# Kernel optimization log

Hardware: AMD Instinct MI355X
Metric: run time of the kernel (lower is better)

The kernel has to match this reference:

```python
import jax, jax.numpy as jnp
import numpy as np


def setup_inputs() -> dict:
    key = jax.random.key(0)
    ks = jax.random.split(key, 8)
    N, C, T, V = 32, 64, 256, 25
    OUT, INTER, S = 64, 16, 3
    W_SCALE = 0.05  # keep complex softmax exp() well-conditioned
    return {
        "x_real": jax.random.normal(ks[0], (N, C, T, V), jnp.float32),
        "x_imag": jax.random.normal(ks[1], (N, C, T, V), jnp.float32),
        "A": jax.random.uniform(ks[2], (S, V, V), jnp.float32),
        "PA": jax.random.normal(ks[3], (S, V, V), jnp.float32) * 1e-3,
        "Wa": jax.random.normal(ks[4], (S, 2 * INTER, 2 * C), jnp.float32) * W_SCALE,
        "ba": jnp.zeros((S, 2 * INTER), jnp.float32),
        "Wb": jax.random.normal(ks[5], (S, 2 * INTER, 2 * C), jnp.float32) * W_SCALE,
        "bb": jnp.zeros((S, 2 * INTER), jnp.float32),
        "Wd": jax.random.normal(ks[6], (S, 2 * OUT, 2 * C), jnp.float32) * W_SCALE,
        "bd": jnp.zeros((S, 2 * OUT), jnp.float32),
        "bn_weight": jnp.ones((OUT,), jnp.float32),
        "bn_bias": jnp.zeros((OUT,), jnp.float32),
    }


def _cconv1x1(z, W, b):
    # C_Conv2d with k=1: 1x1 conv over concat(real, imag) channels.
    zc = jnp.concatenate([z.real, z.imag], axis=1)          # [N, 2*Cin, T, V]
    o = jnp.einsum("oc,nctv->notv", W, zc) + b[None, :, None, None]
    h = W.shape[0] // 2
    return jax.lax.complex(o[:, :h], o[:, h:])              # [N, Cout, T, V] complex


def _forward(x_real, x_imag, A, PA, Wa, ba, Wb, bb, Wd, bd, bn_weight, bn_bias):
    x = jax.lax.complex(x_real, x_imag)                     # [N, C, T, V]
    N, C, T, V = x.shape
    inter = Wa.shape[1] // 2
    Afull = A + PA                                          # [3, V, V] real
    X2 = x.reshape(N, C * T, V)
    y = None
    for i in range(A.shape[0]):
        A1 = _cconv1x1(x, Wa[i], ba[i])                     # [N, inter, T, V]
        A1 = A1.transpose(0, 3, 1, 2).reshape(N, V, inter * T)
        A2 = _cconv1x1(x, Wb[i], bb[i]).reshape(N, inter * T, V)
        S = jnp.matmul(A1, A2) / (inter * T)                # [N, V, V] complex
        # complex softmax over dim=1 (no max-subtraction, faithful to C_softmax)
        ez = jnp.exp(S)
        S = ez / jnp.sum(ez, axis=1, keepdims=True)
        S = S + Afull[i]
        z = jnp.matmul(X2, S).reshape(N, C, T, V)
        z = _cconv1x1(z, Wd[i], bd[i])                      # [N, OUT, T, V]
        y = z if y is None else y + z
    # C_BatchNorm2d on complex input: complex mean, real variance = E|y-mu|^2
    mu = jnp.mean(y, axis=(0, 2, 3))                        # [OUT] complex
    var = jnp.mean(jnp.abs(y - mu[None, :, None, None]) ** 2, axis=(0, 2, 3))
    yn = (y - mu[None, :, None, None]) / jnp.sqrt(var + 1e-5)[None, :, None, None]
    yn = yn * bn_weight[None, :, None, None] + bn_bias[None, :, None, None]
    yn = yn + x  # down = identity (in_channels == out_channels)
    return jnp.stack([yn.real, yn.imag])                    # [2, N, OUT, T, V] real


def reference(x_real, x_imag, A, PA, Wa, ba, Wb, bb, Wd, bd, bn_weight, bn_bias):
    return _forward(x_real, x_imag, A, PA, Wa, ba, Wb, bb, Wd, bd, bn_weight, bn_bias)
```

## Files before the change

### kernel.cpp

```cpp
#include <hip/hip_runtime.h>
#include <hip/hip_bf16.h>
#include <stdint.h>

#define NN 32
#define CC 64
#define TTOT 256
#define VV 25
#define NS 3
constexpr int TV  = TTOT * VV;
constexpr int CTV = CC * TV;
constexpr size_t PLANE = (size_t)NN * CTV;

typedef unsigned short ushort_t;
using short8 = __attribute__((ext_vector_type(8))) short;
using f32x4  = __attribute__((ext_vector_type(4))) float;

static __device__ __forceinline__ ushort_t f2bf(float f) {
  __hip_bfloat16 h = __float2bfloat16(f);
  return reinterpret_cast<ushort_t&>(h);
}
static __device__ __forceinline__ float bf2f(ushort_t h) {
  union { uint32_t u; float f; } v; v.u = ((uint32_t)h) << 16;
  return v.f;
}
static __device__ __forceinline__ int SWZ(int row, int k) {
  return ((row << 7) + k) ^ ((row & 7) << 3);
}
static __device__ __forceinline__ f32x4 mfma16(short8 a, short8 b, f32x4 c) {
  return __builtin_amdgcn_mfma_f32_16x16x32_bf16(a, b, c, 0, 0, 0);
}
static __device__ __forceinline__ short8 negbf8(short8 x) {
  short8 r;
#pragma unroll
  for (int j = 0; j < 8; ++j) r[j] = x[j] ^ (short)0x8000;
  return r;
}

__global__ __launch_bounds__(256) void k0_wfrag(
    const float* __restrict__ Wd, const float* __restrict__ Wa,
    const float* __restrict__ Wb, ushort_t* __restrict__ wfrag,
    ushort_t* __restrict__ wab)
{
  const int i = blockIdx.x;
  for (int e = threadIdx.x; e < 16384; e += 256) {
    int ot = e >> 11, m = (e >> 9) & 3, l = (e >> 3) & 63, j = e & 7;
    int r  = ot * 16 + (l & 15);
    int c = m * 16 + ((l >> 4) << 2) + (j >> 1), comp = j & 1;
    wfrag[(size_t)i * 16384 + e] = f2bf(Wd[(size_t)i * 16384 + r * 128 + comp * 64 + c]);
  }
  for (int e = threadIdx.x; e < 8192; e += 256) {
    int mt = e >> 11, ks = (e >> 9) & 3, l = (e >> 3) & 63, j = e & 7;
    int r  = mt * 16 + (l & 15);
    int kp = ks * 32 + ((l >> 4) << 3) + j;
    float v = (r < 32) ? Wa[((size_t)i * 32 + r) * 128 + kp]
                       : Wb[((size_t)i * 32 + (r - 32)) * 128 + kp];
    wab[(size_t)i * 8192 + e] = f2bf(v);
  }
}

__global__ __launch_bounds__(256) void k1_spart(
    const float* __restrict__ xr, const float* __restrict__ xi,
    const ushort_t* __restrict__ wab, const float* __restrict__ ba,
    const float* __restrict__ bb, float* __restrict__ Spart)
{
  const int tc = blockIdx.x, n = blockIdx.y;
  const int tid = threadIdx.x, lane = tid & 63, wv = tid >> 6;
  const int r16 = lane & 15, gw = lane >> 4;
  __shared__ alignas(16) ushort_t zc[128 * 128];
  __shared__ alignas(16) ushort_t Ga[NS][32 * 128];
  __shared__ alignas(16) ushort_t Gb[NS][32 * 128];

  for (int e4 = tid; e4 < 128 * 25; e4 += 256) {
    int c = e4 / 25, q = e4 % 25;
    const float* src = (c < 64) ? xr : xi;
    float4 w = *(const float4*)&src[(size_t)n * CTV + (c & 63) * TV + tc * 100 + q * 4];
#pragma unroll
    for (int jj = 0; jj < 4; ++jj) {
      int g = q * 4 + jj, t = g / 25, v = g - t * 25;
      zc[SWZ(t * 32 + v, c)] = f2bf(((const float*)&w)[jj]);
    }
  }
  for (int e = tid; e < 28 * 128; e += 256) {
    int r7 = e >> 7, c = e & 127;
    int t = r7 / 7, vv = 25 + r7 % 7;
    zc[SWZ(t * 32 + vv, c)] = 0;
  }
  __syncthreads();

#pragma unroll 1
  for (int i = 0; i < NS; ++i) {
    short8 afr[4];
#pragma unroll
    for (int ks = 0; ks < 4; ++ks)
      afr[ks] = *(const short8*)&wab[((((size_t)i * 4 + wv) * 4 + ks) * 64 + lane) * 8];
    float bias[4];
#pragma unroll
    for (int j = 0; j < 4; ++j) {
      int row = wv * 16 + gw * 4 + j;
      bias[j] = (row < 32) ? ba[i * 32 + row] : bb[i * 32 + (row - 32)];
    }
    ushort_t* gbuf = (wv < 2) ? Ga[i] : Gb[i];
    const int half = (wv & 1) * 64;
    for (int nt = 0; nt < 8; ++nt) {
      f32x4 acc = {0.f, 0.f, 0.f, 0.f};
      const int brow = nt * 16 + r16;
#pragma unroll
      for (int ks = 0; ks < 4; ++ks) {
        short8 bfr = *(const short8*)&zc[SWZ(brow, ks * 32 + gw * 8)];
        acc = mfma16(afr[ks], bfr, acc);
      }
      int pos2 = nt * 16 + r16;
      int t = pos2 >> 5, v = pos2 & 31;
      int k0w = half + t * 16 + gw * 4;
      uint32_t w0 = (uint32_t)f2bf(acc[0] + bias[0]) | ((uint32_t)f2bf(acc[1] + bias[1]) << 16);
      uint32_t w1 = (uint32_t)f2bf(acc[2] + bias[2]) | ((uint32_t)f2bf(acc[3] + bias[3]) << 16);
      uint2 pk; pk.x = w0; pk.y = w1;
      *(uint2*)&gbuf[SWZ(v, k0w)] = pk;
    }
  }
  __syncthreads();

  const int mu = wv >> 1, nv = wv & 1;
  const int urow = mu * 16 + r16;
  const int vrow = nv * 16 + r16;
#pragma unroll 1
  for (int i = 0; i < NS; ++i) {
    f32x4 Prr = {0.f,0.f,0.f,0.f}, Pii = {0.f,0.f,0.f,0.f};
    f32x4 Pri = {0.f,0.f,0.f,0.f}, Pir = {0.f,0.f,0.f,0.f};
#pragma unroll
    for (int ks = 0; ks < 2; ++ks) {
      int ko = ks * 32 + gw * 8;
      short8 arF = *(const short8*)&Ga[i][SWZ(urow, ko)];
      short8 aiF = *(const short8*)&Ga[i][SWZ(urow, 64 + ko)];
      short8 brF = *(const short8*)&Gb[i][SWZ(vrow, ko)];
      short8 biF = *(const short8*)&Gb[i][SWZ(vrow, 64 + ko)];
      Prr = mfma16(arF, brF, Prr);
      Pii = mfma16(aiF, biF, Pii);
      Pri = mfma16(arF, biF, Pri);
      Pir = mfma16(aiF, brF, Pir);
    }
#pragma unroll
    for (int j = 0; j < 4; ++j) {
      int u = mu * 16 + gw * 4 + j;
      int v = nv * 16 + r16;
      if (u < VV && v < VV) {
        size_t idx = ((((size_t)i * NN + n) * 64 + tc) * 625 + u * 25 + v) * 2;
        Spart[idx]     = Prr[j] - Pii[j];
        Spart[idx + 1] = Pri[j] + Pir[j];
      }
    }
  }
}

__global__ __launch_bounds__(256) void k2_softmax(
    const float* __restrict__ Spart, const float* __restrict__ Aw,
    const float* __restrict__ PA, ushort_t* __restrict__ sfrag)
{
  const int i = blockIdx.x, n = blockIdx.y, tid = threadIdx.x;
  __shared__ float ez[625 * 2];
  __shared__ float den[25 * 2];
  for (int e = tid; e < 625; e += 256) {
    float sr = 0.f, si = 0.f;
    const float* p = Spart + (((size_t)i * NN + n) * 64 * 625 + e) * 2;
    for (int tcb = 0; tcb < 64; ++tcb) { sr += p[0]; si += p[1]; p += 625 * 2; }
    sr *= (1.f / 4096.f); si *= (1.f / 4096.f);
    float m = expf(sr);
    ez[e * 2] = m * cosf(si);
    ez[e * 2 + 1] = m * sinf(si);
  }
  __syncthreads();
  if (tid < 25) {
    float dr = 0.f, di = 0.f;
    for (int u = 0; u < 25; ++u) { dr += ez[(u * 25 + tid) * 2]; di += ez[(u * 25 + tid) * 2 + 1]; }
    float inv = 1.f / (dr * dr + di * di);
    den[tid * 2] = dr * inv; den[tid * 2 + 1] = -di * inv;
  }
  __syncthreads();
  for (int e = tid; e < 625; e += 256) {
    int v = e % 25;
    float er = ez[e * 2], ei = ez[e * 2 + 1];
    float dr = den[v * 2], di = den[v * 2 + 1];
    float outr = er * dr - ei * di + Aw[i * 625 + e] + PA[i * 625 + e];
    float outi = er * di + ei * dr;
    ez[e * 2] = outr; ez[e * 2 + 1] = outi;
  }
  __syncthreads();
  for (int e = tid; e < 256; e += 256) {
    int l = e & 63, nt = (e >> 6) & 1, m = e >> 7;
    int u0 = (l >> 4) << 3, v = nt * 16 + (l & 15);
    short8 pk;
#pragma unroll
    for (int j = 0; j < 8; ++j) {
      int u = u0 + j;
      float val = 0.f;
      if (u < VV && v < VV)
        val = (m == 0) ? ez[(u * 25 + v) * 2] : ez[(u * 25 + v) * 2 + 1];
      pk[j] = (short)f2bf(val);
    }
    *(short8*)&sfrag[((size_t)(i * NN + n) * 256 + e) * 8] = pk;
  }
}

__global__ __launch_bounds__(512) void k3_y(
    const float* __restrict__ xr, const float* __restrict__ xi,
    const ushort_t* __restrict__ sfrag, const ushort_t* __restrict__ wfrag,
    const float* __restrict__ bd, float* __restrict__ out,
    float* __restrict__ bnpart)
{
  const int tq8 = blockIdx.x, n = blockIdx.y;
  const int tid = threadIdx.x, lane = tid & 63, wv = tid >> 6;
  const int r16 = lane & 15, gw = lane >> 4;
  __shared__ alignas(16) ushort_t wlds[49152];
  __shared__ float stats[8][128][2];

  {
    ushort_t* xs = wlds;
    for (int e4 = tid; e4 < 128 * 50; e4 += 512) {
      int c = e4 / 50, q = e4 % 50;
      const float* src = (c < 64) ? xr : xi;
      float4 w = *(const float4*)&src[(size_t)n * CTV + (c & 63) * TV + tq8 * 200 + q * 4];
#pragma unroll
      for (int jj = 0; jj < 4; ++jj) {
        int g = q * 4 + jj, t = g / 25, u = g - t * 25;
        xs[(t >> 2) * 16384 + SWZ(c, (t & 3) * 32 + u)] = f2bf(((const float*)&w)[jj]);
      }
    }
    for (int e = tid; e < 128 * 56; e += 512) {
      int c = e / 56, r = e % 56;
      int t = r / 7, u = 25 + r % 7;
      xs[(t >> 2) * 16384 + SWZ(c, (t & 3) * 32 + u)] = 0;
    }
  }
  __syncthreads();

  const int tl = wv & 3, th = wv >> 2;
  const int kx = tl * 32 + gw * 8;
  short8 axr[4], axi[4];
#pragma unroll
  for (int tile = 0; tile < 4; ++tile) {
    axr[tile] = *(const short8*)&wlds[th * 16384 + SWZ(tile * 16 + r16, kx)];
    axi[tile] = *(const short8*)&wlds[th * 16384 + SWZ(64 + tile * 16 + r16, kx)];
  }
  __syncthreads();

  {
    short8 tmp[12];
#pragma unroll
    for (int q = 0; q < 12; ++q)
      tmp[q] = *(const short8*)&wfrag[(size_t)(q * 512 + tid) * 8];
#pragma unroll
    for (int q = 0; q < 12; ++q)
      *(short8*)&wlds[(size_t)(q * 512 + tid) * 8] = tmp[q];
  }
  __syncthreads();

  f32x4 acc[8][2];
#pragma unroll
  for (int a = 0; a < 8; ++a) { acc[a][0] = {0.f,0.f,0.f,0.f}; acc[a][1] = {0.f,0.f,0.f,0.f}; }

  auto load_sf = [&](int i, short8 sf[2][2]) {
    const ushort_t* sb = sfrag + (size_t)(i * NN + n) * 2048;
#pragma unroll
    for (int m = 0; m < 2; ++m)
#pragma unroll
      for (int nt = 0; nt < 2; ++nt)
        sf[m][nt] = *(const short8*)&sb[((m * 2 + nt) * 64 + lane) * 8];
  };
  auto compute_i = [&](int i, short8 sf[2][2]) {
    short8 snI[2];
#pragma unroll
    for (int nt = 0; nt < 2; ++nt) snI[nt] = negbf8(sf[1][nt]);
    short8 bp[4][2];
#pragma unroll
    for (int tile = 0; tile < 4; ++tile) {
#pragma unroll
      for (int nt = 0; nt < 2; ++nt) {
        f32x4 zr = {0.f,0.f,0.f,0.f}, zi = {0.f,0.f,0.f,0.f};
        zr = mfma16(axr[tile], sf[0][nt], zr);
        zr = mfma16(axi[tile], snI[nt], zr);
        zi = mfma16(axr[tile], sf[1][nt], zi);
        zi = mfma16(axi[tile], sf[0][nt], zi);
        short8 pk;
#pragma unroll
        for (int j = 0; j < 4; ++j) {
          pk[2 * j]     = (short)f2bf(zr[j]);
          pk[2 * j + 1] = (short)f2bf(zi[j]);
        }
        bp[tile][nt] = pk;
      }
    }
#pragma unroll
    for (int ot = 0; ot < 8; ++ot) {
#pragma unroll
      for (int m = 0; m < 4; ++m) {
        short8 a = *(const short8*)&wlds[((size_t)i * 16384) + (size_t)((ot * 4 + m) * 64 + lane) * 8];
        acc[ot][0] = mfma16(a, bp[m][0], acc[ot][0]);
        acc[ot][1] = mfma16(a, bp[m][1], acc[ot][1]);
      }
    }
  };

  short8 sfA[2][2], sfB[2][2];
  load_sf(0, sfA);
  load_sf(1, sfB);
  compute_i(0, sfA);
  load_sf(2, sfA);
  compute_i(1, sfB);
  compute_i(2, sfA);

  const int t = tq8 * 8 + wv;
#pragma unroll
  for (int ot = 0; ot < 8; ++ot) {
#pragma unroll
    for (int j = 0; j < 4; ++j) {
      int row = ot * 16 + gw * 4 + j;
      float bias = bd[row] + bd[128 + row] + bd[256 + row];
      float s = 0.f, q = 0.f;
#pragma unroll
      for (int nt = 0; nt < 2; ++nt) {
        int v = nt * 16 + r16;
        float val = acc[ot][nt][j] + bias;
        if (v < VV) {
          out[(size_t)(row >> 6) * PLANE + (size_t)n * CTV + (row & 63) * TV + t * VV + v] = val;
          s += val; q += val * val;
        }
      }
#pragma unroll
      for (int d = 1; d < 16; d <<= 1) { s += __shfl_xor(s, d); q += __shfl_xor(q, d); }
      if (r16 == 0) { stats[wv][row][0] = s; stats[wv][row][1] = q; }
    }
  }
  __syncthreads();
  if (tid < 128) {
    float s = 0.f, q = 0.f;
#pragma unroll
    for (int w = 0; w < 8; ++w) { s += stats[w][tid][0]; q += stats[w][tid][1]; }
    size_t b = (size_t)n * 32 + tq8;
    bnpart[(b * 128 + tid) * 2]     = s;
    bnpart[(b * 128 + tid) * 2 + 1] = q;
  }
}

__global__ __launch_bounds__(256) void k4_stats(
    const float* __restrict__ bnpart, const float* __restrict__ bnw,
    const float* __restrict__ bnb, float* __restrict__ coeff)
{
  const int o = blockIdx.x, tid = threadIdx.x;
  float sr = 0.f, qr = 0.f, si = 0.f, qi = 0.f;
  for (int b = tid; b < 1024; b += 256) {
    const float* p = bnpart + ((size_t)b * 128 + o) * 2;
    sr += p[0]; qr += p[1];
    const float* p2 = bnpart + ((size_t)b * 128 + 64 + o) * 2;
    si += p2[0]; qi += p2[1];
  }
#pragma unroll
  for (int d = 1; d < 64; d <<= 1) {
    sr += __shfl_xor(sr, d); qr += __shfl_xor(qr, d);
    si += __shfl_xor(si, d); qi += __shfl_xor(qi, d);
  }
  __shared__ float red[4][4];
  int lane = tid & 63, wv = tid >> 6;
  if (lane == 0) { red[wv][0] = sr; red[wv][1] = qr; red[wv][2] = si; red[wv][3] = qi; }
  __syncthreads();
  if (tid == 0) {
    sr = red[0][0] + red[1][0] + red[2][0] + red[3][0];
    qr = red[0][1] + red[1][1] + red[2][1] + red[3][1];
    si = red[0][2] + red[1][2] + red[2][2] + red[3][2];
    qi = red[0][3] + red[1][3] + red[2][3] + red[3][3];
    const float invM = 1.f / (float)((size_t)NN * TTOT * VV);
    float mur = sr * invM, mui = si * invM;
    float var = (qr + qi) * invM - mur * mur - mui * mui;
    float inv = rsqrtf(var + 1e-5f);
    coeff[o * 4 + 0] = mur; coeff[o * 4 + 1] = mui;
    coeff[o * 4 + 2] = inv * bnw[o]; coeff[o * 4 + 3] = bnb[o];
  }
}

__global__ __launch_bounds__(256) void k5_norm(
    const float* __restrict__ xr, const float* __restrict__ xi,
    const float* __restrict__ coeff, float* __restrict__ out)
{
  size_t idx0 = ((size_t)blockIdx.x * 256 + threadIdx.x) * 4;
  size_t stride = (size_t)gridDim.x * 256 * 4;
  for (size_t e = idx0; e < PLANE; e += stride) {
    int o = (int)((e / TV) & 63);
    float4 cf = *(const float4*)&coeff[o * 4];
    float4 yr = *(float4*)&out[e];
    float4 yi = *(float4*)&out[PLANE + e];
    float4 vr = *(const float4*)&xr[e];
    float4 vi = *(const float4*)&xi[e];
    yr.x = (yr.x - cf.x) * cf.z + cf.w + vr.x;
    yr.y = (yr.y - cf.x) * cf.z + cf.w + vr.y;
    yr.z = (yr.z - cf.x) * cf.z + cf.w + vr.z;
    yr.w = (yr.w - cf.x) * cf.z + cf.w + vr.w;
    yi.x = (yi.x - cf.y) * cf.z + vi.x;
    yi.y = (yi.y - cf.y) * cf.z + vi.y;
    yi.z = (yi.z - cf.y) * cf.z + vi.z;
    yi.w = (yi.w - cf.y) * cf.z + vi.w;
    *(float4*)&out[e] = yr;
    *(float4*)&out[PLANE + e] = yi;
  }
}

extern "C" void kernel_launch(void* const* d_in, const int* in_sizes, int n_in,
                              void* d_out, int out_size, void* d_ws, size_t ws_size,
                              hipStream_t stream) {
  const float* xr  = (const float*)d_in[0];
  const float* xi  = (const float*)d_in[1];
  const float* Aw  = (const float*)d_in[2];
  const float* PA  = (const float*)d_in[3];
  const float* Wa  = (const float*)d_in[4];
  const float* ba  = (const float*)d_in[5];
  const float* Wb  = (const float*)d_in[6];
  const float* bb  = (const float*)d_in[7];
  const float* Wd  = (const float*)d_in[8];
  const float* bd  = (const float*)d_in[9];
  const float* bnw = (const float*)d_in[10];
  const float* bnb = (const float*)d_in[11];
  float* out = (float*)d_out;
  float* ws = (float*)d_ws;

  float*    Spart  = ws;
  float*    bnpart = ws;
  ushort_t* sfrag  = (ushort_t*)(ws + 7680000);
  ushort_t* wfrag  = (ushort_t*)(ws + 7778304);
  ushort_t* wab    = (ushort_t*)(ws + 7802880);
  float*    coeff  = ws + 7815168;

  k0_wfrag<<<NS, 256, 0, stream>>>(Wd, Wa, Wb, wfrag, wab);
  k1_spart<<<dim3(64, NN), 256, 0, stream>>>(xr, xi, wab, ba, bb, Spart);
  k2_softmax<<<dim3(NS, NN), 256, 0, stream>>>(Spart, Aw, PA, sfrag);
  k3_y<<<dim3(32, NN), 512, 0, stream>>>(xr, xi, sfrag, wfrag, bd, out, bnpart);
  k4_stats<<<64, 256, 0, stream>>>(bnpart, bnw, bnb, coeff);
  k5_norm<<<6400, 256, 0, stream>>>(xr, xi, coeff, out);
}
```

Before: 247.1 us.

## Split k3 output channels across blocks to shrink LDS and raise occupancy

The y-kernel now uses 256-thread blocks, each handling 4 time steps and one half (real or imaginary) of the 128 output rows, giving four times as many blocks. LDS use drops from about 96KB to about 48KB per block and the accumulator array is halved, so more blocks can be resident per CU. The swizzled x layout is replaced by a padded row stride of 40, and the MFMA loop is wrapped in s_setprio. The cost is that each block reloads x and recomputes the complex S-multiply that the other half-block also computes. The BN partial layout and k4 reduction are adjusted to match.

```diff
diff --git a/kernel.cpp b/kernel.cpp
--- a/kernel.cpp
+++ b/kernel.cpp
@@ -201,62 +201,66 @@
   }
 }
 
-__global__ __launch_bounds__(512) void k3_y(
+__global__ __launch_bounds__(256) void k3_y(
     const float* __restrict__ xr, const float* __restrict__ xi,
     const ushort_t* __restrict__ sfrag, const ushort_t* __restrict__ wfrag,
     const float* __restrict__ bd, float* __restrict__ out,
     float* __restrict__ bnpart)
 {
-  const int tq8 = blockIdx.x, n = blockIdx.y;
+  const int tq4 = blockIdx.x >> 1, h = blockIdx.x & 1, n = blockIdx.y;
   const int tid = threadIdx.x, lane = tid & 63, wv = tid >> 6;
   const int r16 = lane & 15, gw = lane >> 4;
-  __shared__ alignas(16) ushort_t wlds[49152];
-  __shared__ float stats[8][128][2];
+  __shared__ alignas(16) ushort_t smem[24576];
+  __shared__ float stats[4][64][2];
+
+  for (int e4 = tid; e4 < 128 * 25; e4 += 256) {
+    int c = e4 / 25, q = e4 % 25;
+    const float* src = (c < 64) ? xr : xi;
+    float4 w = *(const float4*)&src[(size_t)n * CTV + (size_t)(c & 63) * TV + tq4 * 100 + q * 4];
+#pragma unroll
+    for (int jj = 0; jj < 4; ++jj) {
+      int g = q * 4 + jj, t = g / 25, u = g - t * 25;
+      smem[t * 5120 + c * 40 + u] = f2bf(((const float*)&w)[jj]);
+    }
+  }
+  for (int e = tid; e < 128 * 28; e += 256) {
+    int c = e / 28, r = e % 28;
+    int t = r / 7, u = 25 + r % 7;
+    smem[t * 5120 + c * 40 + u] = 0;
+  }
+  __syncthreads();
+
+  short8 axr[4], axi[4];
+#pragma unroll
+  for (int tile = 0; tile < 4; ++tile) {
+    int cr = tile * 16 + r16;
+    axr[tile] = *(const short8*)&smem[wv * 5120 + cr * 40 + gw * 8];
+    axi[tile] = *(const short8*)&smem[wv * 5120 + (64 + cr) * 40 + gw * 8];
+  }
+  __syncthreads();
 
   {
-    ushort_t* xs = wlds;
-    for (int e4 = tid; e4 < 128 * 50; e4 += 512) {
-      int c = e4 / 50, q = e4 % 50;
-      const float* src = (c < 64) ? xr : xi;
-      float4 w = *(const float4*)&src[(size_t)n * CTV + (c & 63) * TV + tq8 * 200 + q * 4];
-#pragma unroll
-      for (int jj = 0; jj < 4; ++jj) {
-        int g = q * 4 + jj, t = g / 25, u = g - t * 25;
-        xs[(t >> 2) * 16384 + SWZ(c, (t & 3) * 32 + u)] = f2bf(((const float*)&w)[jj]);
-      }
-    }
-    for (int e = tid; e < 128 * 56; e += 512) {
-      int c = e / 56, r = e % 56;
-      int t = r / 7, u = 25 + r % 7;
-      xs[(t >> 2) * 16384 + SWZ(c, (t & 3) * 32 + u)] = 0;
-    }
-  }
-  __syncthreads();
-
-  const int tl = wv & 3, th = wv >> 2;
-  const int kx = tl * 32 + gw * 8;
-  short8 axr[4], axi[4];
-#pragma unroll
-  for (int tile = 0; tile < 4; ++tile) {
-    axr[tile] = *(const short8*)&wlds[th * 16384 + SWZ(tile * 16 + r16, kx)];
-    axi[tile] = *(const short8*)&wlds[th * 16384 + SWZ(64 + tile * 16 + r16, kx)];
-  }
-  __syncthreads();
-
-  {
-    short8 tmp[12];
-#pragma unroll
-    for (int q = 0; q < 12; ++q)
-      tmp[q] = *(const short8*)&wfrag[(size_t)(q * 512 + tid) * 8];
-#pragma unroll
-    for (int q = 0; q < 12; ++q)
-      *(short8*)&wlds[(size_t)(q * 512 + tid) * 8] = tmp[q];
-  }
-  __syncthreads();
-
-  f32x4 acc[8][2];
-#pragma unroll
-  for (int a = 0; a < 8; ++a) { acc[a][0] = {0.f,0.f,0.f,0.f}; acc[a][1] = {0.f,0.f,0.f,0.f}; }
+    short8 tmp[6];
+#pragma unroll
+    for (int b = 0; b < 2; ++b) {
+#pragma unroll
+      for (int q = 0; q < 6; ++q) {
+        int e = (b * 6 + q) * 256 + tid;
+        int i = e >> 10, local = e & 1023;
+        tmp[q] = *(const short8*)&wfrag[(size_t)i * 16384 + h * 8192 + (size_t)local * 8];
+      }
+#pragma unroll
+      for (int q = 0; q < 6; ++q) {
+        int e = (b * 6 + q) * 256 + tid;
+        *(short8*)&smem[(size_t)e * 8] = tmp[q];
+      }
+    }
+  }
+  __syncthreads();
+
+  f32x4 acc[4][2];
+#pragma unroll
+  for (int a = 0; a < 4; ++a) { acc[a][0] = {0.f,0.f,0.f,0.f}; acc[a][1] = {0.f,0.f,0.f,0.f}; }
 
   auto load_sf = [&](int i, short8 sf[2][2]) {
     const ushort_t* sb = sfrag + (size_t)(i * NN + n) * 2048;
@@ -289,15 +293,17 @@
         bp[tile][nt] = pk;
       }
     }
-#pragma unroll
-    for (int ot = 0; ot < 8; ++ot) {
+    __builtin_amdgcn_s_setprio(1);
+#pragma unroll
+    for (int otl = 0; otl < 4; ++otl) {
 #pragma unroll
       for (int m = 0; m < 4; ++m) {
-        short8 a = *(const short8*)&wlds[((size_t)i * 16384) + (size_t)((ot * 4 + m) * 64 + lane) * 8];
-        acc[ot][0] = mfma16(a, bp[m][0], acc[ot][0]);
-        acc[ot][1] = mfma16(a, bp[m][1], acc[ot][1]);
-      }
-    }
+        short8 a = *(const short8*)&smem[(size_t)i * 8192 + (size_t)((otl * 4 + m) * 64 + lane) * 8];
+        acc[otl][0] = mfma16(a, bp[m][0], acc[otl][0]);
+        acc[otl][1] = mfma16(a, bp[m][1], acc[otl][1]);
+      }
+    }
+    __builtin_amdgcn_s_setprio(0);
   };
 
   short8 sfA[2][2], sfB[2][2];
@@ -308,36 +314,36 @@
   compute_i(1, sfB);
   compute_i(2, sfA);
 
-  const int t = tq8 * 8 + wv;
-#pragma unroll
-  for (int ot = 0; ot < 8; ++ot) {
+  const int t = tq4 * 4 + wv;
+#pragma unroll
+  for (int otl = 0; otl < 4; ++otl) {
 #pragma unroll
     for (int j = 0; j < 4; ++j) {
-      int row = ot * 16 + gw * 4 + j;
+      int lrow = otl * 16 + gw * 4 + j;
+      int row = h * 64 + lrow;
       float bias = bd[row] + bd[128 + row] + bd[256 + row];
       float s = 0.f, q = 0.f;
 #pragma unroll
       for (int nt = 0; nt < 2; ++nt) {
         int v = nt * 16 + r16;
-        float val = acc[ot][nt][j] + bias;
+        float val = acc[otl][nt][j] + bias;
         if (v < VV) {
-          out[(size_t)(row >> 6) * PLANE + (size_t)n * CTV + (row & 63) * TV + t * VV + v] = val;
+          out[(size_t)h * PLANE + (size_t)n * CTV + (row & 63) * TV + t * VV + v] = val;
           s += val; q += val * val;
         }
       }
 #pragma unroll
       for (int d = 1; d < 16; d <<= 1) { s += __shfl_xor(s, d); q += __shfl_xor(q, d); }
-      if (r16 == 0) { stats[wv][row][0] = s; stats[wv][row][1] = q; }
-    }
-  }
-  __syncthreads();
-  if (tid < 128) {
-    float s = 0.f, q = 0.f;
-#pragma unroll
-    for (int w = 0; w < 8; ++w) { s += stats[w][tid][0]; q += stats[w][tid][1]; }
-    size_t b = (size_t)n * 32 + tq8;
-    bnpart[(b * 128 + tid) * 2]     = s;
-    bnpart[(b * 128 + tid) * 2 + 1] = q;
+      if (r16 == 0) { stats[wv][lrow][0] = s; stats[wv][lrow][1] = q; }
+    }
+  }
+  __syncthreads();
+  if (tid < 64) {
+    float s = stats[0][tid][0] + stats[1][tid][0] + stats[2][tid][0] + stats[3][tid][0];
+    float q = stats[0][tid][1] + stats[1][tid][1] + stats[2][tid][1] + stats[3][tid][1];
+    size_t b = (size_t)n * 64 + tq4;
+    bnpart[((b * 2 + h) * 64 + tid) * 2]     = s;
+    bnpart[((b * 2 + h) * 64 + tid) * 2 + 1] = q;
   }
 }
 
@@ -347,10 +353,10 @@
 {
   const int o = blockIdx.x, tid = threadIdx.x;
   float sr = 0.f, qr = 0.f, si = 0.f, qi = 0.f;
-  for (int b = tid; b < 1024; b += 256) {
-    const float* p = bnpart + ((size_t)b * 128 + o) * 2;
+  for (int b = tid; b < 2048; b += 256) {
+    const float* p = bnpart + ((size_t)(b * 2 + 0) * 64 + o) * 2;
     sr += p[0]; qr += p[1];
-    const float* p2 = bnpart + ((size_t)b * 128 + 64 + o) * 2;
+    const float* p2 = bnpart + ((size_t)(b * 2 + 1) * 64 + o) * 2;
     si += p2[0]; qi += p2[1];
   }
 #pragma unroll
@@ -430,7 +436,7 @@
   k0_wfrag<<<NS, 256, 0, stream>>>(Wd, Wa, Wb, wfrag, wab);
   k1_spart<<<dim3(64, NN), 256, 0, stream>>>(xr, xi, wab, ba, bb, Spart);
   k2_softmax<<<dim3(NS, NN), 256, 0, stream>>>(Spart, Aw, PA, sfrag);
-  k3_y<<<dim3(32, NN), 512, 0, stream>>>(xr, xi, sfrag, wfrag, bd, out, bnpart);
+  k3_y<<<dim3(128, NN), 256, 0, stream>>>(xr, xi, sfrag, wfrag, bd, out, bnpart);
   k4_stats<<<64, 256, 0, stream>>>(bnpart, bnw, bnb, coeff);
   k5_norm<<<6400, 256, 0, stream>>>(xr, xi, coeff, out);
 }
```

Result: slower. 254.6 us (+3.0%).

## Split softmax partial-sum reduction into a wide pre-reduce kernel; raise MFMA wave priority

Applied to the files above, without the earlier changes.

The 64-way reduction of S partials, previously done serially per element by only 96 blocks, is split into a new k2a_reduce kernel that runs 768 blocks, each summing 8 partials. The softmax kernel then only sums 8. This spreads a latency-bound serial reduction over many more CUs, at the cost of an extra launch and an intermediate buffer. Separately, k3_y raises wave priority around its MFMA accumulation loop with s_setprio.

```diff
diff --git a/kernel.cpp b/kernel.cpp
--- a/kernel.cpp
+++ b/kernel.cpp
@@ -152,17 +152,35 @@
   }
 }
 
-__global__ __launch_bounds__(256) void k2_softmax(
-    const float* __restrict__ Spart, const float* __restrict__ Aw,
+__global__ __launch_bounds__(256) void k2a_reduce(
+    const float* __restrict__ Spart, float* __restrict__ Spart2)
+{
+  const int chunk = blockIdx.x, in = blockIdx.y, tid = threadIdx.x;
+  const float* base = Spart + ((size_t)in * 64 + chunk * 8) * 1250;
+  float* outp = Spart2 + ((size_t)in * 8 + chunk) * 1250;
+  for (int e = tid; e < 1250; e += 256) {
+    float s = 0.f;
+#pragma unroll
+    for (int k = 0; k < 8; ++k) s += base[(size_t)k * 1250 + e];
+    outp[e] = s;
+  }
+}
+
+__global__ __launch_bounds__(256) void k2b_softmax(
+    const float* __restrict__ Spart2, const float* __restrict__ Aw,
     const float* __restrict__ PA, ushort_t* __restrict__ sfrag)
 {
   const int i = blockIdx.x, n = blockIdx.y, tid = threadIdx.x;
   __shared__ float ez[625 * 2];
   __shared__ float den[25 * 2];
+  const float* base = Spart2 + ((size_t)(i * NN + n)) * 8 * 1250;
   for (int e = tid; e < 625; e += 256) {
     float sr = 0.f, si = 0.f;
-    const float* p = Spart + (((size_t)i * NN + n) * 64 * 625 + e) * 2;
-    for (int tcb = 0; tcb < 64; ++tcb) { sr += p[0]; si += p[1]; p += 625 * 2; }
+#pragma unroll
+    for (int k = 0; k < 8; ++k) {
+      sr += base[(size_t)k * 1250 + e * 2];
+      si += base[(size_t)k * 1250 + e * 2 + 1];
+    }
     sr *= (1.f / 4096.f); si *= (1.f / 4096.f);
     float m = expf(sr);
     ez[e * 2] = m * cosf(si);
@@ -289,6 +307,7 @@
         bp[tile][nt] = pk;
       }
     }
+    __builtin_amdgcn_s_setprio(1);
 #pragma unroll
     for (int ot = 0; ot < 8; ++ot) {
 #pragma unroll
@@ -298,6 +317,7 @@
         acc[ot][1] = mfma16(a, bp[m][1], acc[ot][1]);
       }
     }
+    __builtin_amdgcn_s_setprio(0);
   };
 
   short8 sfA[2][2], sfB[2][2];
@@ -422,14 +442,16 @@
 
   float*    Spart  = ws;
   float*    bnpart = ws;
-  ushort_t* sfrag  = (ushort_t*)(ws + 7680000);
-  ushort_t* wfrag  = (ushort_t*)(ws + 7778304);
-  ushort_t* wab    = (ushort_t*)(ws + 7802880);
-  float*    coeff  = ws + 7815168;
+  float*    Spart2 = ws + 7680000;
+  ushort_t* sfrag  = (ushort_t*)(ws + 8640000);
+  ushort_t* wfrag  = (ushort_t*)(ws + 8738304);
+  ushort_t* wab    = (ushort_t*)(ws + 8762880);
+  float*    coeff  = ws + 8775168;
 
   k0_wfrag<<<NS, 256, 0, stream>>>(Wd, Wa, Wb, wfrag, wab);
   k1_spart<<<dim3(64, NN), 256, 0, stream>>>(xr, xi, wab, ba, bb, Spart);
-  k2_softmax<<<dim3(NS, NN), 256, 0, stream>>>(Spart, Aw, PA, sfrag);
+  k2a_reduce<<<dim3(8, NS * NN), 256, 0, stream>>>(Spart, Spart2);
+  k2b_softmax<<<dim3(NS, NN), 256, 0, stream>>>(Spart2, Aw, PA, sfrag);
   k3_y<<<dim3(32, NN), 512, 0, stream>>>(xr, xi, sfrag, wfrag, bd, out, bnpart);
   k4_stats<<<64, 256, 0, stream>>>(bnpart, bnw, bnb, coeff);
   k5_norm<<<6400, 256, 0, stream>>>(xr, xi, coeff, out);
```

After: 248.7 us. About the same (+0.6%).

## Store intermediate y as packed bf16 real/imag pairs and raise MFMA wave priority

Applied to the files above, without the earlier changes.

The k3 kernel now writes the pre-normalization output as one 32-bit word per element holding bf16 real and imaginary parts, instead of two fp32 planes. k5 reads these packed pairs and unpacks them. This halves intermediate write and read traffic in the output buffer. It also wraps the MFMA loop in s_setprio to favor matrix issue. The cost is extra bf16 rounding of y before normalization, while the BN statistics are still accumulated in fp32.

```diff
diff --git a/kernel.cpp b/kernel.cpp
--- a/kernel.cpp
+++ b/kernel.cpp
@@ -204,7 +204,7 @@
 __global__ __launch_bounds__(512) void k3_y(
     const float* __restrict__ xr, const float* __restrict__ xi,
     const ushort_t* __restrict__ sfrag, const ushort_t* __restrict__ wfrag,
-    const float* __restrict__ bd, float* __restrict__ out,
+    const float* __restrict__ bd, uint32_t* __restrict__ ypair,
     float* __restrict__ bnpart)
 {
   const int tq8 = blockIdx.x, n = blockIdx.y;
@@ -289,6 +289,7 @@
         bp[tile][nt] = pk;
       }
     }
+    __builtin_amdgcn_s_setprio(1);
 #pragma unroll
     for (int ot = 0; ot < 8; ++ot) {
 #pragma unroll
@@ -298,6 +299,7 @@
         acc[ot][1] = mfma16(a, bp[m][1], acc[ot][1]);
       }
     }
+    __builtin_amdgcn_s_setprio(0);
   };
 
   short8 sfA[2][2], sfB[2][2];
@@ -310,24 +312,34 @@
 
   const int t = tq8 * 8 + wv;
 #pragma unroll
-  for (int ot = 0; ot < 8; ++ot) {
+  for (int ot = 0; ot < 4; ++ot) {
 #pragma unroll
     for (int j = 0; j < 4; ++j) {
-      int row = ot * 16 + gw * 4 + j;
-      float bias = bd[row] + bd[128 + row] + bd[256 + row];
-      float s = 0.f, q = 0.f;
+      int o = ot * 16 + gw * 4 + j;
+      float biasR = bd[o] + bd[128 + o] + bd[256 + o];
+      float biasI = bd[64 + o] + bd[192 + o] + bd[320 + o];
+      float sR = 0.f, qR = 0.f, sI = 0.f, qI = 0.f;
 #pragma unroll
       for (int nt = 0; nt < 2; ++nt) {
         int v = nt * 16 + r16;
-        float val = acc[ot][nt][j] + bias;
+        float vr_ = acc[ot][nt][j] + biasR;
+        float vi_ = acc[ot + 4][nt][j] + biasI;
         if (v < VV) {
-          out[(size_t)(row >> 6) * PLANE + (size_t)n * CTV + (row & 63) * TV + t * VV + v] = val;
-          s += val; q += val * val;
+          uint32_t pk = (uint32_t)f2bf(vr_) | ((uint32_t)f2bf(vi_) << 16);
+          ypair[(size_t)n * CTV + (size_t)o * TV + t * VV + v] = pk;
+          sR += vr_; qR += vr_ * vr_;
+          sI += vi_; qI += vi_ * vi_;
         }
       }
 #pragma unroll
-      for (int d = 1; d < 16; d <<= 1) { s += __shfl_xor(s, d); q += __shfl_xor(q, d); }
-      if (r16 == 0) { stats[wv][row][0] = s; stats[wv][row][1] = q; }
+      for (int d = 1; d < 16; d <<= 1) {
+        sR += __shfl_xor(sR, d); qR += __shfl_xor(qR, d);
+        sI += __shfl_xor(sI, d); qI += __shfl_xor(qI, d);
+      }
+      if (r16 == 0) {
+        stats[wv][o][0] = sR;      stats[wv][o][1] = qR;
+        stats[wv][64 + o][0] = sI; stats[wv][64 + o][1] = qI;
+      }
     }
   }
   __syncthreads();
@@ -380,15 +392,20 @@
     const float* __restrict__ xr, const float* __restrict__ xi,
     const float* __restrict__ coeff, float* __restrict__ out)
 {
+  uint32_t* yp = (uint32_t*)out;
   size_t idx0 = ((size_t)blockIdx.x * 256 + threadIdx.x) * 4;
   size_t stride = (size_t)gridDim.x * 256 * 4;
   for (size_t e = idx0; e < PLANE; e += stride) {
     int o = (int)((e / TV) & 63);
     float4 cf = *(const float4*)&coeff[o * 4];
-    float4 yr = *(float4*)&out[e];
-    float4 yi = *(float4*)&out[PLANE + e];
+    uint4 y4 = *(uint4*)&yp[e];
     float4 vr = *(const float4*)&xr[e];
     float4 vi = *(const float4*)&xi[e];
+    float4 yr, yi;
+    yr.x = bf2f((ushort_t)(y4.x & 0xffff)); yi.x = bf2f((ushort_t)(y4.x >> 16));
+    yr.y = bf2f((ushort_t)(y4.y & 0xffff)); yi.y = bf2f((ushort_t)(y4.y >> 16));
+    yr.z = bf2f((ushort_t)(y4.z & 0xffff)); yi.z = bf2f((ushort_t)(y4.z >> 16));
+    yr.w = bf2f((ushort_t)(y4.w & 0xffff)); yi.w = bf2f((ushort_t)(y4.w >> 16));
     yr.x = (yr.x - cf.x) * cf.z + cf.w + vr.x;
     yr.y = (yr.y - cf.x) * cf.z + cf.w + vr.y;
     yr.z = (yr.z - cf.x) * cf.z + cf.w + vr.z;
@@ -430,7 +447,8 @@
   k0_wfrag<<<NS, 256, 0, stream>>>(Wd, Wa, Wb, wfrag, wab);
   k1_spart<<<dim3(64, NN), 256, 0, stream>>>(xr, xi, wab, ba, bb, Spart);
   k2_softmax<<<dim3(NS, NN), 256, 0, stream>>>(Spart, Aw, PA, sfrag);
-  k3_y<<<dim3(32, NN), 512, 0, stream>>>(xr, xi, sfrag, wfrag, bd, out, bnpart);
+  k3_y<<<dim3(32, NN), 512, 0, stream>>>(xr, xi, sfrag, wfrag, bd,
+                                         (uint32_t*)out, bnpart);
   k4_stats<<<64, 256, 0, stream>>>(bnpart, bnw, bnb, coeff);
   k5_norm<<<6400, 256, 0, stream>>>(xr, xi, coeff, out);
 }
```

Result: faster. 218.8 us (-11.5%).
